# Kernel optimization log

Hardware: AMD Instinct MI355X
Metric: run time of the kernel (lower is better)

## Reference

```python
import jax, jax.numpy as jnp
import numpy as np

N, E, F_IN, F_OUT = 8192, 1024, 256, 256


def setup_inputs() -> dict:
    key = jax.random.key(0)
    k1, k2, k3, k4 = jax.random.split(key, 4)
    X = jax.random.normal(k1, (N, F_IN), dtype=jnp.float32)
    # binary incidence matrix: node i belongs to hyperedge j with p=0.05
    H = (jax.random.uniform(k2, (N, E)) < 0.05).astype(jnp.float32)
    W = jax.random.normal(k3, (F_OUT, F_IN), dtype=jnp.float32) * (1.0 / np.sqrt(F_IN))
    b = jax.random.normal(k4, (F_OUT,), dtype=jnp.float32) * 0.01
    return {"X": X, "H": H, "W": W, "b": b}


def reference(X, H, W, b):
    # Dv = diag(row sums of H), De = diag(col sums of H)
    dv = jnp.sum(H, axis=1)                      # [N] node degrees
    de = jnp.sum(H, axis=0)                      # [E] edge degrees
    dv_inv_sqrt = 1.0 / jnp.sqrt(dv)             # inv of sqrt(Dv) (diagonal)
    de_inv = 1.0 / de                            # inv of De (diagonal)
    # diagonal matrices realized as broadcast scalings (same math, no N x N).
    Xs = X * dv_inv_sqrt[:, None]
    M = H.T @ Xs                                 # H^T (...)          [E, F]
    M = M * de_inv[:, None]                      # De^-1 (...)        [E, F]
    X_new = (H @ M) * dv_inv_sqrt[:, None]       # Dv^-1/2 H (...)    [N, F]
    return X_new @ W.T + b                       # nn.Linear
```

## Files before the change

kernel.cpp:

```cpp
#include <hip/hip_runtime.h>
#include <hip/hip_bf16.h>
#include <stdint.h>

typedef __attribute__((ext_vector_type(8))) short bf16x8;
typedef __attribute__((ext_vector_type(4))) float f32x4;
typedef __attribute__((ext_vector_type(4))) unsigned int u32x4;
typedef __attribute__((ext_vector_type(2))) unsigned int u32x2;
typedef unsigned short u16;
typedef unsigned int u32;
typedef unsigned long long u64;

#define N_NODES 8192
#define N_EDGES 1024
#define F_DIM   256
#define NMAX 128
#define EMAX 512
#define NSEG 256

__device__ __forceinline__ u16 f2bf(float f) {
    union { float f; u32 u; } v; v.f = f;
    u32 u = v.u;
    u = (u + 0x7FFFu + ((u >> 16) & 1u)) >> 16;
    return (u16)u;
}
__device__ __forceinline__ float bflo(u32 p) {
    union { u32 u; float f; } v; v.u = p << 16; return v.f;
}
__device__ __forceinline__ float bfhi(u32 p) {
    union { u32 u; float f; } v; v.u = p & 0xffff0000u; return v.f;
}

__global__ __launch_bounds__(512) void prep(
    const float* __restrict__ H, const float* __restrict__ X,
    const float* __restrict__ W,
    float* __restrict__ dv, u16* __restrict__ nlist,
    u16* __restrict__ Xs, u32* __restrict__ HbT, u16* __restrict__ Wb) {
    __shared__ u16 hmask[32][64];
    const int tid = threadIdx.x;
    const int wv = tid >> 6;
    const int lane = tid & 63;
    const int blk = blockIdx.x;
    const int n0 = blk * 32 + wv * 4;

    f32x4 hv[4][4], xv[4];
#pragma unroll
    for (int r = 0; r < 4; ++r) {
        const int n = n0 + r;
#pragma unroll
        for (int q = 0; q < 4; ++q)
            hv[r][q] = *(const f32x4*)(&H[(size_t)n * N_EDGES + q * 256 + lane * 4]);
        xv[r] = *(const f32x4*)(&X[(size_t)n * F_DIM + lane * 4]);
    }

    if (wv == 7) {
        const f32x4 w = *(const f32x4*)(&W[(size_t)blk * F_DIM + lane * 4]);
        u32x2 pk;
        pk[0] = (u32)f2bf(w[0]) | ((u32)f2bf(w[1]) << 16);
        pk[1] = (u32)f2bf(w[2]) | ((u32)f2bf(w[3]) << 16);
        *(u32x2*)(&Wb[(size_t)blk * F_DIM + lane * 4]) = pk;
    }

#pragma unroll
    for (int r = 0; r < 4; ++r) {
        const int n = n0 + r;
        u32 m16 = 0u;
#pragma unroll
        for (int q = 0; q < 4; ++q)
#pragma unroll
            for (int j = 0; j < 4; ++j)
                m16 |= ((hv[r][q][j] != 0.f) ? 1u : 0u) << (q * 4 + j);
        hmask[wv * 4 + r][lane] = (u16)m16;
        const u32 cl = (u32)__popc(m16);
        u32 x = cl;
#pragma unroll
        for (int d = 1; d < 64; d <<= 1) {
            const u32 t = __shfl_up(x, d, 64);
            if (lane >= d) x += t;
        }
        const u32 total = __shfl(x, 63, 64);
        u32 pos = x - cl;
        u16* nrow = &nlist[(size_t)n * NMAX];
        u32 m = m16;
        while (m) {
            const int bidx = __builtin_ctz(m);
            m &= m - 1;
            const int col = ((bidx >> 2) << 8) + lane * 4 + (bidx & 3);
            if (pos < NMAX) nrow[pos] = (u16)col;
            ++pos;
        }
        if (lane == 0) dv[n] = (float)total;
        const float s = rsqrtf((float)total);
        u32x2 pk;
        pk[0] = (u32)f2bf(xv[r][0] * s) | ((u32)f2bf(xv[r][1] * s) << 16);
        pk[1] = (u32)f2bf(xv[r][2] * s) | ((u32)f2bf(xv[r][3] * s) << 16);
        *(u32x2*)(&Xs[(size_t)n * F_DIM + lane * 4]) = pk;
    }
    __syncthreads();
#pragma unroll
    for (int eo = 0; eo < 2; ++eo) {
        const int e = tid + eo * 512;
        const int widx = (e & 255) >> 2;
        const int bit = ((e >> 8) << 2) + (e & 3);
        u32 w = 0u;
#pragma unroll
        for (int r = 0; r < 32; ++r)
            w |= (u32)((hmask[r][widx] >> bit) & 1u) << r;
        HbT[(size_t)e * NSEG + blk] = w;
    }
}

__global__ __launch_bounds__(512) void spmm1(
    const u16* __restrict__ Xs, const u32* __restrict__ HbT,
    u16* __restrict__ Mb) {
    __shared__ u32 words[NSEG];
    __shared__ u16 lst[EMAX];
    __shared__ u32 wtot[4];
    __shared__ float red[16][2][128];
    const int tid = threadIdx.x;
    const int wv = tid >> 6;
    const int lane = tid & 63;
    const int e = blockIdx.x;
    if (tid < NSEG) words[tid] = HbT[(size_t)e * NSEG + tid];
    __syncthreads();
    u32 c = 0, x = 0;
    if (tid < NSEG) {
        c = (u32)__popc(words[tid]);
        x = c;
#pragma unroll
        for (int d = 1; d < 64; d <<= 1) {
            const u32 t = __shfl_up(x, d, 64);
            if (lane >= d) x += t;
        }
        if (lane == 63) wtot[wv] = x;
    }
    __syncthreads();
    if (tid < NSEG) {
        u32 off = 0;
        for (int w = 0; w < wv; ++w) off += wtot[w];
        u32 pos = off + x - c;
        u32 m = words[tid];
        const int nb = tid * 32;
        while (m) {
            const int b = __builtin_ctz(m);
            m &= m - 1;
            if (pos < EMAX) lst[pos] = (u16)(nb + b);
            ++pos;
        }
    }
    __syncthreads();
    const u32 de = wtot[0] + wtot[1] + wtot[2] + wtot[3];
    const int cnt = min((int)de, EMAX);
    const int half = lane >> 5, l32 = lane & 31;
    const int npairs = (cnt + 1) >> 1;
    const int len = (npairs + 7) >> 3;
    const int p0 = wv * len;
    const int p1 = min(p0 + len, npairs);
    float a[8] = {};
#pragma unroll 8
    for (int p = p0; p < p1; ++p) {
        const int idx0 = 2 * p + half;
        const int idx = min(idx0, cnt - 1);
        const float msk = (idx0 < cnt) ? 1.f : 0.f;
        const int n = lst[idx];
        const u32x4 pk = *(const u32x4*)(&Xs[(size_t)n * F_DIM + l32 * 8]);
        a[0] = fmaf(bflo(pk[0]), msk, a[0]); a[1] = fmaf(bfhi(pk[0]), msk, a[1]);
        a[2] = fmaf(bflo(pk[1]), msk, a[2]); a[3] = fmaf(bfhi(pk[1]), msk, a[3]);
        a[4] = fmaf(bflo(pk[2]), msk, a[4]); a[5] = fmaf(bfhi(pk[2]), msk, a[5]);
        a[6] = fmaf(bflo(pk[3]), msk, a[6]); a[7] = fmaf(bfhi(pk[3]), msk, a[7]);
    }
    const int ws = wv * 2 + half;
    f32x4 r0 = {a[0], a[1], a[2], a[3]};
    f32x4 r1 = {a[4], a[5], a[6], a[7]};
    *(f32x4*)(&red[ws][0][l32 * 4]) = r0;
    *(f32x4*)(&red[ws][1][l32 * 4]) = r1;
    __syncthreads();
    if (tid < F_DIM) {
        const int f = tid;
        const int pl = (f >> 2) & 1;
        const int ix = ((f >> 3) << 2) | (f & 3);
        float s = 0.f;
#pragma unroll
        for (int w = 0; w < 16; ++w) s += red[w][pl][ix];
        Mb[(size_t)e * F_DIM + f] = f2bf(s / (float)de);
    }
}

__global__ __launch_bounds__(512) void spmm2w(
    const u16* __restrict__ Mb, const float* __restrict__ dv,
    const u16* __restrict__ nlist, const u16* __restrict__ Wb,
    const float* __restrict__ bias, float* __restrict__ out) {
    __shared__ u16 nl[8 * NMAX];
    __shared__ u16 Yb[8][264];
    const int tid = threadIdx.x;
    const int wv = tid >> 6;
    const int lane = tid & 63;
    const int n0 = blockIdx.x * 8;
    ((u32*)nl)[tid] = ((const u32*)&nlist[(size_t)n0 * NMAX])[tid];
    __syncthreads();
    const int half = lane >> 5, l32 = lane & 31;
    const int n = n0 + wv;
    const float dvn = dv[n];
    const int cnt = min((int)dvn, NMAX);
    const u16* lt = &nl[wv * NMAX];
    float a[8] = {};
    const int npairs = (cnt + 1) >> 1;
#pragma unroll 8
    for (int p = 0; p < npairs; ++p) {
        const int idx0 = 2 * p + half;
        const int idx = min(idx0, cnt - 1);
        const float msk = (idx0 < cnt) ? 1.f : 0.f;
        const int e = lt[idx];
        const u32x4 pk = *(const u32x4*)(&Mb[(size_t)e * F_DIM + l32 * 8]);
        a[0] = fmaf(bflo(pk[0]), msk, a[0]); a[1] = fmaf(bfhi(pk[0]), msk, a[1]);
        a[2] = fmaf(bflo(pk[1]), msk, a[2]); a[3] = fmaf(bfhi(pk[1]), msk, a[3]);
        a[4] = fmaf(bflo(pk[2]), msk, a[4]); a[5] = fmaf(bfhi(pk[2]), msk, a[5]);
        a[6] = fmaf(bflo(pk[3]), msk, a[6]); a[7] = fmaf(bfhi(pk[3]), msk, a[7]);
    }
#pragma unroll
    for (int k = 0; k < 8; ++k) a[k] += __shfl_xor(a[k], 32, 64);
    const float s = rsqrtf(dvn);
    if (half == 0) {
        u32x4 pk;
        pk[0] = (u32)f2bf(a[0] * s) | ((u32)f2bf(a[1] * s) << 16);
        pk[1] = (u32)f2bf(a[2] * s) | ((u32)f2bf(a[3] * s) << 16);
        pk[2] = (u32)f2bf(a[4] * s) | ((u32)f2bf(a[5] * s) << 16);
        pk[3] = (u32)f2bf(a[6] * s) | ((u32)f2bf(a[7] * s) << 16);
        *(u32x4*)(&Yb[wv][l32 * 8]) = pk;
    }
    __syncthreads();
    const int row16 = lane & 15, quad = lane >> 4;
    f32x4 acc[2] = {};
    for (int ko = 0; ko < 256; ko += 32) {
        bf16x8 af = {};
        if (row16 < 8)
            af = *(const bf16x8*)(&Yb[row16][ko + quad * 8]);
#pragma unroll
        for (int tn = 0; tn < 2; ++tn) {
            const int j = wv * 32 + tn * 16 + row16;
            const bf16x8 bf = *(const bf16x8*)(&Wb[(size_t)j * F_DIM + ko + quad * 8]);
            acc[tn] = __builtin_amdgcn_mfma_f32_16x16x32_bf16(af, bf, acc[tn], 0, 0, 0);
        }
    }
#pragma unroll
    for (int tn = 0; tn < 2; ++tn) {
        const int col = wv * 32 + tn * 16 + row16;
        const float bc = bias[col];
#pragma unroll
        for (int r2 = 0; r2 < 4; ++r2) {
            const int row = quad * 4 + r2;
            if (row < 8)
                out[(size_t)(n0 + row) * F_DIM + col] = acc[tn][r2] + bc;
        }
    }
}

extern "C" void kernel_launch(void* const* d_in, const int* in_sizes, int n_in,
                              void* d_out, int out_size, void* d_ws, size_t ws_size,
                              hipStream_t stream) {
    (void)in_sizes; (void)n_in; (void)out_size; (void)ws_size;
    const float* X = (const float*)d_in[0];
    const float* H = (const float*)d_in[1];
    const float* W = (const float*)d_in[2];
    const float* b = (const float*)d_in[3];
    float* out = (float*)d_out;

    char* ws = (char*)d_ws;
    float* dv    = (float*)(ws);
    u32*   HbT   = (u32*)(ws + 0x10000);
    u16*   nlist = (u16*)(ws + 0x110000);
    u16*   Xs    = (u16*)(ws + 0x310000);
    u16*   Mb    = (u16*)(ws + 0x710000);
    u16*   Wb    = (u16*)(ws + 0x790000);

    prep<<<NSEG, 512, 0, stream>>>(H, X, W, dv, nlist, Xs, HbT, Wb);
    spmm1<<<N_EDGES, 512, 0, stream>>>(Xs, HbT, Mb);
    spmm2w<<<N_NODES / 8, 512, 0, stream>>>(Mb, dv, nlist, Wb, b, out);
}
```

Before: 134.4 us.

## Split spmm1 feature dimension across two blocks per hyperedge

spmm1 now launches two blocks per hyperedge, each handling 128 of the 256 features. Each wave processes four member nodes at once with 16 lanes per node instead of two nodes with 32 lanes. The cross-wave reduction and the bf16 output store change to match. The aim is more parallelism and shorter per-block gather loops, at the cost of each block rebuilding the member list from the bitmask, which doubles that work and the HbT reads.

```diff
diff --git a/kernel.cpp b/kernel.cpp
--- a/kernel.cpp
+++ b/kernel.cpp
@@ -115,11 +115,12 @@
     __shared__ u32 words[NSEG];
     __shared__ u16 lst[EMAX];
     __shared__ u32 wtot[4];
-    __shared__ float red[16][2][128];
+    __shared__ float red[32][132];
     const int tid = threadIdx.x;
     const int wv = tid >> 6;
     const int lane = tid & 63;
-    const int e = blockIdx.x;
+    const int e = blockIdx.x & (N_EDGES - 1);
+    const int fbase = (blockIdx.x >> 10) * 128;
     if (tid < NSEG) words[tid] = HbT[(size_t)e * NSEG + tid];
     __syncthreads();
     u32 c = 0, x = 0;
@@ -150,38 +151,38 @@
     __syncthreads();
     const u32 de = wtot[0] + wtot[1] + wtot[2] + wtot[3];
     const int cnt = min((int)de, EMAX);
-    const int half = lane >> 5, l32 = lane & 31;
-    const int npairs = (cnt + 1) >> 1;
-    const int len = (npairs + 7) >> 3;
+    const int quad = lane >> 4, l16 = lane & 15;
+    const int nq = (cnt + 3) >> 2;
+    const int len = (nq + 7) >> 3;
     const int p0 = wv * len;
-    const int p1 = min(p0 + len, npairs);
+    const int p1 = min(p0 + len, nq);
     float a[8] = {};
 #pragma unroll 8
     for (int p = p0; p < p1; ++p) {
-        const int idx0 = 2 * p + half;
+        const int idx0 = p * 4 + quad;
         const int idx = min(idx0, cnt - 1);
         const float msk = (idx0 < cnt) ? 1.f : 0.f;
         const int n = lst[idx];
-        const u32x4 pk = *(const u32x4*)(&Xs[(size_t)n * F_DIM + l32 * 8]);
+        const u32x4 pk = *(const u32x4*)(&Xs[(size_t)n * F_DIM + fbase + l16 * 8]);
         a[0] = fmaf(bflo(pk[0]), msk, a[0]); a[1] = fmaf(bfhi(pk[0]), msk, a[1]);
         a[2] = fmaf(bflo(pk[1]), msk, a[2]); a[3] = fmaf(bfhi(pk[1]), msk, a[3]);
         a[4] = fmaf(bflo(pk[2]), msk, a[4]); a[5] = fmaf(bfhi(pk[2]), msk, a[5]);
         a[6] = fmaf(bflo(pk[3]), msk, a[6]); a[7] = fmaf(bfhi(pk[3]), msk, a[7]);
     }
-    const int ws = wv * 2 + half;
+    const int ws = wv * 4 + quad;
     f32x4 r0 = {a[0], a[1], a[2], a[3]};
     f32x4 r1 = {a[4], a[5], a[6], a[7]};
-    *(f32x4*)(&red[ws][0][l32 * 4]) = r0;
-    *(f32x4*)(&red[ws][1][l32 * 4]) = r1;
-    __syncthreads();
-    if (tid < F_DIM) {
-        const int f = tid;
-        const int pl = (f >> 2) & 1;
-        const int ix = ((f >> 3) << 2) | (f & 3);
-        float s = 0.f;
-#pragma unroll
-        for (int w = 0; w < 16; ++w) s += red[w][pl][ix];
-        Mb[(size_t)e * F_DIM + f] = f2bf(s / (float)de);
+    *(f32x4*)(&red[ws][l16 * 8]) = r0;
+    *(f32x4*)(&red[ws][l16 * 8 + 4]) = r1;
+    __syncthreads();
+    if (tid < 64) {
+        const int f0 = tid * 2;
+        float s0 = 0.f, s1 = 0.f;
+#pragma unroll
+        for (int w = 0; w < 32; ++w) { s0 += red[w][f0]; s1 += red[w][f0 + 1]; }
+        const float dei = 1.f / (float)de;
+        const u32 pk = (u32)f2bf(s0 * dei) | ((u32)f2bf(s1 * dei) << 16);
+        *(u32*)(&Mb[(size_t)e * F_DIM + fbase + f0]) = pk;
     }
 }
 
@@ -273,6 +274,6 @@
     u16*   Wb    = (u16*)(ws + 0x790000);
 
     prep<<<NSEG, 512, 0, stream>>>(H, X, W, dv, nlist, Xs, HbT, Wb);
-    spmm1<<<N_EDGES, 512, 0, stream>>>(Xs, HbT, Mb);
+    spmm1<<<2 * N_EDGES, 512, 0, stream>>>(Xs, HbT, Mb);
     spmm2w<<<N_NODES / 8, 512, 0, stream>>>(Mb, dv, nlist, Wb, b, out);
 }
```

Result: slower. 138.1 us (+2.8%).

## Replace gather-based H^T X SpMM with dense bit-expanded bf16 MFMA GEMM

Applied to the files above, without the earlier changes.

The first sparse aggregation, which built a per-edge node list and gathered rows of Xs, is replaced by a dense MFMA GEMM over the full incidence bitmask. The bits are expanded to bf16 0/1 operands on the fly, and a transposed Xs is streamed through LDS with async global-to-LDS loads and a 4-stage buffer. The prep kernel now writes Xs transposed and the bitmask in a node-segment-major layout to feed it. This trades irregular gathers and per-edge list building for about 20x more dense arithmetic, and it uses only 512 single-wave blocks, so parallelism is low.

```diff
diff --git a/kernel.cpp b/kernel.cpp
--- a/kernel.cpp
+++ b/kernel.cpp
@@ -14,8 +14,6 @@
 #define N_EDGES 1024
 #define F_DIM   256
 #define NMAX 128
-#define EMAX 512
-#define NSEG 256
 
 __device__ __forceinline__ u16 f2bf(float f) {
     union { float f; u32 u; } v; v.f = f;
@@ -30,12 +28,28 @@
     union { u32 u; float f; } v; v.u = p & 0xffff0000u; return v.f;
 }
 
+__device__ __forceinline__ void async16(const u16* g, u16* l) {
+    __builtin_amdgcn_global_load_lds(
+        (const __attribute__((address_space(1))) u32*)(const void*)g,
+        (__attribute__((address_space(3))) u32*)(void*)l, 16, 0, 0);
+}
+
+__device__ __forceinline__ bf16x8 expand8(u32 byte) {
+    union { u32 u[4]; bf16x8 v; } r;
+#pragma unroll
+    for (int i = 0; i < 4; ++i)
+        r.u[i] = (((byte >> (2 * i)) & 1u) ? 0x3F80u : 0u)
+               | (((byte >> (2 * i + 1)) & 1u) ? 0x3F800000u : 0u);
+    return r.v;
+}
+
 __global__ __launch_bounds__(512) void prep(
     const float* __restrict__ H, const float* __restrict__ X,
     const float* __restrict__ W,
     float* __restrict__ dv, u16* __restrict__ nlist,
-    u16* __restrict__ Xs, u32* __restrict__ HbT, u16* __restrict__ Wb) {
+    u16* __restrict__ Xst, u32* __restrict__ HbTs, u16* __restrict__ Wb) {
     __shared__ u16 hmask[32][64];
+    __shared__ u16 tT[256][34];
     const int tid = threadIdx.x;
     const int wv = tid >> 6;
     const int lane = tid & 63;
@@ -90,98 +104,103 @@
         }
         if (lane == 0) dv[n] = (float)total;
         const float s = rsqrtf((float)total);
-        u32x2 pk;
-        pk[0] = (u32)f2bf(xv[r][0] * s) | ((u32)f2bf(xv[r][1] * s) << 16);
-        pk[1] = (u32)f2bf(xv[r][2] * s) | ((u32)f2bf(xv[r][3] * s) << 16);
-        *(u32x2*)(&Xs[(size_t)n * F_DIM + lane * 4]) = pk;
+#pragma unroll
+        for (int j = 0; j < 4; ++j)
+            tT[lane * 4 + j][wv * 4 + r] = f2bf(xv[r][j] * s);
     }
     __syncthreads();
-#pragma unroll
-    for (int eo = 0; eo < 2; ++eo) {
-        const int e = tid + eo * 512;
-        const int widx = (e & 255) >> 2;
-        const int bit = ((e >> 8) << 2) + (e & 3);
-        u32 w = 0u;
-#pragma unroll
-        for (int r = 0; r < 32; ++r)
-            w |= (u32)((hmask[r][widx] >> bit) & 1u) << r;
-        HbT[(size_t)e * NSEG + blk] = w;
-    }
-}
-
-__global__ __launch_bounds__(512) void spmm1(
-    const u16* __restrict__ Xs, const u32* __restrict__ HbT,
+    {
+        u32x2 st;
+#pragma unroll
+        for (int eo = 0; eo < 2; ++eo) {
+            const int e = tid * 2 + eo;
+            const int widx = (e & 255) >> 2;
+            const int bit = ((e >> 8) << 2) + (e & 3);
+            u32 w = 0u;
+#pragma unroll
+            for (int r = 0; r < 32; ++r)
+                w |= (u32)((hmask[r][widx] >> bit) & 1u) << r;
+            st[eo] = w;
+        }
+        *(u32x2*)(&HbTs[(size_t)blk * N_EDGES + tid * 2]) = st;
+    }
+    {
+        const int f = tid & 255, half = tid >> 8;
+        const u32* src = (const u32*)(&tT[f][half * 16]);
+        u32x4 a, b2;
+#pragma unroll
+        for (int i = 0; i < 4; ++i) { a[i] = src[i]; b2[i] = src[i + 4]; }
+        u16* dst = &Xst[(size_t)f * N_NODES + blk * 32 + half * 16];
+        *(u32x4*)dst = a;
+        *(u32x4*)(dst + 8) = b2;
+    }
+}
+
+__global__ __launch_bounds__(64) void gemm1(
+    const u16* __restrict__ Xst, const u32* __restrict__ HbTs,
     u16* __restrict__ Mb) {
-    __shared__ u32 words[NSEG];
-    __shared__ u16 lst[EMAX];
-    __shared__ u32 wtot[4];
-    __shared__ float red[16][2][128];
-    const int tid = threadIdx.x;
-    const int wv = tid >> 6;
-    const int lane = tid & 63;
-    const int e = blockIdx.x;
-    if (tid < NSEG) words[tid] = HbT[(size_t)e * NSEG + tid];
-    __syncthreads();
-    u32 c = 0, x = 0;
-    if (tid < NSEG) {
-        c = (u32)__popc(words[tid]);
-        x = c;
-#pragma unroll
-        for (int d = 1; d < 64; d <<= 1) {
-            const u32 t = __shfl_up(x, d, 64);
-            if (lane >= d) x += t;
-        }
-        if (lane == 63) wtot[wv] = x;
-    }
-    __syncthreads();
-    if (tid < NSEG) {
-        u32 off = 0;
-        for (int w = 0; w < wv; ++w) off += wtot[w];
-        u32 pos = off + x - c;
-        u32 m = words[tid];
-        const int nb = tid * 32;
-        while (m) {
-            const int b = __builtin_ctz(m);
-            m &= m - 1;
-            if (pos < EMAX) lst[pos] = (u16)(nb + b);
-            ++pos;
-        }
-    }
-    __syncthreads();
-    const u32 de = wtot[0] + wtot[1] + wtot[2] + wtot[3];
-    const int cnt = min((int)de, EMAX);
-    const int half = lane >> 5, l32 = lane & 31;
-    const int npairs = (cnt + 1) >> 1;
-    const int len = (npairs + 7) >> 3;
-    const int p0 = wv * len;
-    const int p1 = min(p0 + len, npairs);
-    float a[8] = {};
-#pragma unroll 8
-    for (int p = p0; p < p1; ++p) {
-        const int idx0 = 2 * p + half;
-        const int idx = min(idx0, cnt - 1);
-        const float msk = (idx0 < cnt) ? 1.f : 0.f;
-        const int n = lst[idx];
-        const u32x4 pk = *(const u32x4*)(&Xs[(size_t)n * F_DIM + l32 * 8]);
-        a[0] = fmaf(bflo(pk[0]), msk, a[0]); a[1] = fmaf(bfhi(pk[0]), msk, a[1]);
-        a[2] = fmaf(bflo(pk[1]), msk, a[2]); a[3] = fmaf(bfhi(pk[1]), msk, a[3]);
-        a[4] = fmaf(bflo(pk[2]), msk, a[4]); a[5] = fmaf(bfhi(pk[2]), msk, a[5]);
-        a[6] = fmaf(bflo(pk[3]), msk, a[6]); a[7] = fmaf(bfhi(pk[3]), msk, a[7]);
-    }
-    const int ws = wv * 2 + half;
-    f32x4 r0 = {a[0], a[1], a[2], a[3]};
-    f32x4 r1 = {a[4], a[5], a[6], a[7]};
-    *(f32x4*)(&red[ws][0][l32 * 4]) = r0;
-    *(f32x4*)(&red[ws][1][l32 * 4]) = r1;
-    __syncthreads();
-    if (tid < F_DIM) {
-        const int f = tid;
-        const int pl = (f >> 2) & 1;
-        const int ix = ((f >> 3) << 2) | (f & 3);
-        float s = 0.f;
-#pragma unroll
-        for (int w = 0; w < 16; ++w) s += red[w][pl][ix];
-        Mb[(size_t)e * F_DIM + f] = f2bf(s / (float)de);
+    __shared__ u16 Bs[4][16][64];
+    __shared__ float des[32];
+    const int lane = threadIdx.x;
+    const int e0 = (blockIdx.x & 31) * 32;
+    const int f0 = (blockIdx.x >> 5) * 16;
+    const int row16 = lane & 15, quad = lane >> 4;
+    const int srow = lane >> 3;
+    const int schunk = lane & 7;
+    const u16* gB0 = Xst + (size_t)(f0 + srow) * N_NODES + (schunk ^ (srow & 7)) * 8;
+    const u16* gB1 = gB0 + (size_t)8 * N_NODES;
+
+    f32x4 acc[2] = {};
+    u32 cnt0 = 0, cnt1 = 0;
+
+#define STAGE(c)  { const int _b = (c) & 3; const size_t _o = (size_t)(c) * 64; \
+                    async16(gB0 + _o, (u16*)&Bs[_b][0][0]); \
+                    async16(gB1 + _o, (u16*)&Bs[_b][8][0]); }
+#define LOADW(c, w) { _Pragma("unroll") \
+                      for (int _eh = 0; _eh < 2; ++_eh) { _Pragma("unroll") \
+                      for (int _ks = 0; _ks < 2; ++_ks) \
+                          w[_eh][_ks] = HbTs[(size_t)((c) * 2 + _ks) * N_EDGES + e0 + _eh * 16 + row16]; } }
+#define PROCESS(w, bsel) { \
+        asm volatile("s_waitcnt vmcnt(6)" ::: "memory"); \
+        _Pragma("unroll") \
+        for (int _ks = 0; _ks < 2; ++_ks) { \
+            const bf16x8 _bf = *(const bf16x8*)(&Bs[bsel][row16][(((_ks * 4 + quad) ^ (row16 & 7)) * 8)]); \
+            const u32 _b0 = (w[0][_ks] >> (quad * 8)) & 0xFFu; \
+            const u32 _b1 = (w[1][_ks] >> (quad * 8)) & 0xFFu; \
+            cnt0 += (u32)__popc(_b0); cnt1 += (u32)__popc(_b1); \
+            acc[0] = __builtin_amdgcn_mfma_f32_16x16x32_bf16(expand8(_b0), _bf, acc[0], 0, 0, 0); \
+            acc[1] = __builtin_amdgcn_mfma_f32_16x16x32_bf16(expand8(_b1), _bf, acc[1], 0, 0, 0); \
+        } }
+
+    u32 wA[2][2], wB[2][2];
+    STAGE(0); STAGE(1);
+    LOADW(0, wA);
+    for (int it = 0; it < 128; it += 2) {
+        STAGE(min(it + 2, 127));
+        LOADW(min(it + 1, 127), wB);
+        PROCESS(wA, (it & 3));
+        STAGE(min(it + 3, 127));
+        LOADW(min(it + 2, 127), wA);
+        PROCESS(wB, ((it + 1) & 3));
+    }
+#undef STAGE
+#undef LOADW
+#undef PROCESS
+
+    cnt0 += __shfl_down(cnt0, 32, 64); cnt0 += __shfl_down(cnt0, 16, 64);
+    cnt1 += __shfl_down(cnt1, 32, 64); cnt1 += __shfl_down(cnt1, 16, 64);
+    if (lane < 16) {
+        des[lane] = 1.f / (float)cnt0;
+        des[16 + lane] = 1.f / (float)cnt1;
+    }
+#pragma unroll
+    for (int eh = 0; eh < 2; ++eh) {
+        const int col = f0 + row16;
+#pragma unroll
+        for (int r = 0; r < 4; ++r) {
+            const int el = eh * 16 + quad * 4 + r;
+            Mb[(size_t)(e0 + el) * F_DIM + col] = f2bf(acc[eh][r] * des[el]);
+        }
     }
 }
 
@@ -266,13 +285,13 @@
 
     char* ws = (char*)d_ws;
     float* dv    = (float*)(ws);
-    u32*   HbT   = (u32*)(ws + 0x10000);
+    u32*   HbTs  = (u32*)(ws + 0x10000);
     u16*   nlist = (u16*)(ws + 0x110000);
-    u16*   Xs    = (u16*)(ws + 0x310000);
+    u16*   Xst   = (u16*)(ws + 0x310000);
     u16*   Mb    = (u16*)(ws + 0x710000);
     u16*   Wb    = (u16*)(ws + 0x790000);
 
-    prep<<<NSEG, 512, 0, stream>>>(H, X, W, dv, nlist, Xs, HbT, Wb);
-    spmm1<<<N_EDGES, 512, 0, stream>>>(Xs, HbT, Mb);
+    prep<<<256, 512, 0, stream>>>(H, X, W, dv, nlist, Xst, HbTs, Wb);
+    gemm1<<<512, 64, 0, stream>>>(Xst, HbTs, Mb);
     spmm2w<<<N_NODES / 8, 512, 0, stream>>>(Mb, dv, nlist, Wb, b, out);
 }
```

Measured after the change: 175.1 us. +30.3%, slower.
